# Performance work log

Measured on AMD Instinct MI355X. Metric: run time of the kernel, lower is better.

Reference implementation:

```python
import jax, jax.numpy as jnp
import numpy as np

EMBED_DIM = 1024
NUM_HEADS = 16
D_K = EMBED_DIM // NUM_HEADS


def setup_inputs() -> dict:
    key = jax.random.key(0)
    ks = jax.random.split(key, 5)
    x = jax.random.normal(ks[0], (2, 2048, EMBED_DIM), dtype=jnp.float32)
    # kaiming_normal on 2D params: std = sqrt(2/fan_in) with fan_in = in_features
    w_qkv = jax.random.normal(ks[1], (3 * EMBED_DIM, EMBED_DIM), dtype=jnp.float32) * np.sqrt(2.0 / EMBED_DIM)
    b_qkv = jnp.zeros((3 * EMBED_DIM,), dtype=jnp.float32)
    w_o = jax.random.normal(ks[2], (EMBED_DIM, EMBED_DIM), dtype=jnp.float32) * np.sqrt(2.0 / EMBED_DIM)
    b_o = jnp.zeros((EMBED_DIM,), dtype=jnp.float32)
    return {"x": x, "w_qkv": w_qkv, "b_qkv": b_qkv, "w_o": w_o, "b_o": b_o}


def reference(x, w_qkv, b_qkv, w_o, b_o):
    B, N, C = x.shape
    qkv = x @ w_qkv.T + b_qkv  # [B,N,3C]
    q, k, v = jnp.split(qkv, 3, axis=-1)
    # [B,H,N,d_k]
    q = q.reshape(B, N, NUM_HEADS, D_K).transpose(0, 2, 1, 3)
    k = k.reshape(B, N, NUM_HEADS, D_K).transpose(0, 2, 1, 3)
    v = v.reshape(B, N, NUM_HEADS, D_K).transpose(0, 2, 1, 3)
    # NOTE: original forward scales by 1/sqrt(embed_dim), not 1/sqrt(d_k)
    scores = jnp.einsum('bhqd,bhkd->bhqk', q, k) / np.sqrt(C).astype(np.float32)
    causal = jnp.tril(jnp.ones((N, N), dtype=bool))
    scores = jnp.where(causal, scores, -jnp.inf)
    attn = jax.nn.softmax(scores, axis=-1)
    out = jnp.einsum('bhqk,bhkd->bhqd', attn, v)  # [B,H,N,d_k]
    out = out.transpose(0, 2, 1, 3).reshape(B, N, C)
    return out @ w_o.T + b_o
```

## Files before the change

kernel.cpp:

```cpp
#include <hip/hip_runtime.h>
#include <hip/hip_bf16.h>
#include <math.h>

typedef __bf16 bf16_t;
typedef __bf16 bf16x8 __attribute__((ext_vector_type(8)));
typedef __bf16 bf16x4 __attribute__((ext_vector_type(4)));
typedef __bf16 bf16x2 __attribute__((ext_vector_type(2)));
typedef float f32x4 __attribute__((ext_vector_type(4)));
typedef unsigned u32x4 __attribute__((ext_vector_type(4)));

#define SCALE_L2E 0.045084234f
#define ROUND_B 0.0028169f

#define MFMA16(a, b, c) __builtin_amdgcn_mfma_f32_16x16x32_bf16(a, b, c, 0, 0, 0)

__device__ __forceinline__ unsigned pack2(float a, float b) {
  return __builtin_amdgcn_perm(__builtin_bit_cast(unsigned, b),
                               __builtin_bit_cast(unsigned, a), 0x07060302u);
}

__global__ void convert3_f32_bf16(const float* __restrict__ a, int na,
                                  const float* __restrict__ b, int nb,
                                  const float* __restrict__ c, int nc,
                                  bf16_t* __restrict__ oa, bf16_t* __restrict__ ob,
                                  bf16_t* __restrict__ oc) {
  int i = (blockIdx.x * blockDim.x + threadIdx.x) * 8;
  const float* src;
  bf16_t* dst;
  int off;
  if (i < na) { src = a; dst = oa; off = i; }
  else if (i < na + nb) { src = b; dst = ob; off = i - na; }
  else if (i < na + nb + nc) { src = c; dst = oc; off = i - na - nb; }
  else return;
  float4 u = *(const float4*)&src[off];
  float4 v = *(const float4*)&src[off + 4];
  bf16x8 w = {(bf16_t)u.x, (bf16_t)u.y, (bf16_t)u.z, (bf16_t)u.w,
              (bf16_t)v.x, (bf16_t)v.y, (bf16_t)v.z, (bf16_t)v.w};
  *(bf16x8*)&dst[off] = w;
}

#define GLOBAL_AS __attribute__((address_space(1)))
#define LDS_AS __attribute__((address_space(3)))
__device__ __forceinline__ void g2l16(const void* g, void* l) {
  __builtin_amdgcn_global_load_lds((const GLOBAL_AS void*)g, (LDS_AS void*)l,
                                   16, 0, 0);
}

template <typename TC, int BN>
__launch_bounds__(256)
__global__ void gemm_bt_bias(const bf16_t* __restrict__ A,
                             const bf16_t* __restrict__ B,
                             const float* __restrict__ bias,
                             TC* __restrict__ C,
                             int M, int N, int K) {
  constexpr int NT = BN / 32;
  __shared__ bf16_t As[128 * 32];
  __shared__ bf16_t Bs[BN * 32];

  const int t = threadIdx.x;
  const int wave = t >> 6, lane = t & 63, quad = lane >> 4, ln = lane & 15;
  const int wm = (wave >> 1) * 64, wn = (wave & 1) * (BN / 2);
  const int m0 = blockIdx.y * 128, n0 = blockIdx.x * BN;

  const int srow = lane >> 2;
  const int schunk = ((lane & 3) ^ ((lane >> 3) & 3)) * 8;
  const bf16_t* gA0 = &A[(size_t)(m0 + wave * 32 + srow) * K + schunk];
  const bf16_t* gA1 = gA0 + (size_t)16 * K;
  bf16_t* lA0 = &As[(wave * 32) * 32];
  bf16_t* lA1 = &As[(wave * 32 + 16) * 32];
  const bf16_t* gB0 = &B[(size_t)(n0 + (BN == 128 ? wave * 32 : wave * 16) + srow) * K + schunk];
  const bf16_t* gB1 = gB0 + (size_t)16 * K;
  bf16_t* lB0 = &Bs[((BN == 128 ? wave * 32 : wave * 16)) * 32];
  bf16_t* lB1 = &Bs[(wave * 32 + 16) * 32];

  const int cslot = (quad ^ ((ln >> 1) & 3)) * 8;

  f32x4 acc[4][NT];
  for (int i = 0; i < 4; i++)
    for (int j = 0; j < NT; j++) acc[i][j] = (f32x4){0.f, 0.f, 0.f, 0.f};

  for (int k0 = 0; k0 < K; k0 += 32) {
    __syncthreads();
    g2l16(gA0 + k0, lA0);
    g2l16(gA1 + k0, lA1);
    g2l16(gB0 + k0, lB0);
    if (BN == 128) g2l16(gB1 + k0, lB1);
    __syncthreads();

    bf16x8 af[4], bfr[NT];
    for (int mt = 0; mt < 4; mt++)
      af[mt] = *(const bf16x8*)&As[(wm + mt * 16 + ln) * 32 + cslot];
    for (int nt = 0; nt < NT; nt++)
      bfr[nt] = *(const bf16x8*)&Bs[(wn + nt * 16 + ln) * 32 + cslot];
    for (int mt = 0; mt < 4; mt++)
      for (int nt = 0; nt < NT; nt++)
        acc[mt][nt] = MFMA16(af[mt], bfr[nt], acc[mt][nt]);
  }

  for (int nt = 0; nt < NT; nt++) {
    int col = n0 + wn + nt * 16 + ln;
    float bv = bias[col];
    for (int mt = 0; mt < 4; mt++) {
      int row = m0 + wm + mt * 16 + quad * 4;
      for (int r = 0; r < 4; r++)
        C[(size_t)(row + r) * N + col] = (TC)(acc[mt][nt][r] + bv);
    }
  }
}

__launch_bounds__(256, 2)
__global__ void attn_kernel(const bf16_t* __restrict__ qkv,
                            bf16_t* __restrict__ out) {
  constexpr int KP = 72, VP = 72;
  constexpr int BUF = 64 * KP;
  __shared__ __align__(16) bf16_t KsB[2 * BUF];
  __shared__ __align__(16) bf16_t VtB[2 * BUF];

  const int t = threadIdx.x;
  const int wave = t >> 6, lane = t & 63, quad = lane >> 4, ln = lane & 15;
  const int p = blockIdx.x & 15;
  const int bh = blockIdx.x >> 4;
  const int b = bh >> 4, h = bh & 15;
  const int qA = p * 64, qB = (31 - p) * 64;
  const int ntiles = 32 - p;
  const size_t rs = 3072;
  const size_t base = (size_t)b * 2048 * rs;

  const size_t qoffA = base + (size_t)(qA + wave * 16 + ln) * rs + h * 64;
  const size_t qoffB = base + (size_t)(qB + wave * 16 + ln) * rs + h * 64;
  bf16x8 qfA0 = *(const bf16x8*)&qkv[qoffA + quad * 8];
  bf16x8 qfA1 = *(const bf16x8*)&qkv[qoffA + 32 + quad * 8];
  bf16x8 qfB0 = *(const bf16x8*)&qkv[qoffB + quad * 8];
  bf16x8 qfB1 = *(const bf16x8*)&qkv[qoffB + 32 + quad * 8];

  f32x4 oA[4], oB[4];
  float lAx = 0.f, lBx = 0.f;
  for (int ct = 0; ct < 4; ct++) {
    oA[ct] = (f32x4){0.f, 0.f, 0.f, 0.f};
    oB[ct] = (f32x4){0.f, 0.f, 0.f, 0.f};
  }

  const int r0 = t >> 3, c0 = (t & 7) * 8;
  const int ksA = r0 * KP + (((t & 7) + wave) & 7) * 8;
  const int ksB2 = (r0 + 32) * KP + (((t & 7) + wave + 4) & 7) * 8;
  const int vkoff = ((((r0 >> 2) + (t & 7)) & 7)) * 8 + 2 * (r0 & 3);

  const bf16_t* kpa = &qkv[base + 1024 + h * 64 + (size_t)r0 * rs + c0];
  const bf16_t* kpb = kpa + (size_t)32 * rs;
  const bf16_t* vpa = &qkv[base + 2048 + h * 64 + (size_t)(2 * r0) * rs + c0];
  const bf16_t* vpb = vpa + rs;
  const size_t tstep = (size_t)64 * rs;

  bf16x8 ka = *(const bf16x8*)kpa; kpa += tstep;
  bf16x8 kb = *(const bf16x8*)kpb; kpb += tstep;
  bf16x8 va2 = *(const bf16x8*)vpa; vpa += tstep;
  bf16x8 vb2 = *(const bf16x8*)vpb; vpb += tstep;

  const int qgA = qA + wave * 16 + ln;
  const int qgB = qB + wave * 16 + ln;

  auto stage_to = [&](int buf) {
    bf16_t* KsW = &KsB[buf * BUF];
    bf16_t* VtW = &VtB[buf * BUF];
    *(bf16x8*)&KsW[ksA] = ka;
    *(bf16x8*)&KsW[ksB2] = kb;
#pragma unroll
    for (int j = 0; j < 8; j++) {
      bf16x2 w2 = {va2[j], vb2[j]};
      *(bf16x2*)&VtW[(c0 + j) * VP + vkoff] = w2;
    }
  };
  auto prefetch = [&]() {
    ka = *(const bf16x8*)kpa; kpa += tstep;
    kb = *(const bf16x8*)kpb; kpb += tstep;
    va2 = *(const bf16x8*)vpa; vpa += tstep;
    vb2 = *(const bf16x8*)vpb; vpb += tstep;
  };
  auto load_kfs = [&](const bf16_t* Ks, bf16x8* kf0s, bf16x8* kf1s) {
#pragma unroll
    for (int st = 0; st < 4; st++) {
      const int krow = st * 16 + ln;
      const int rot = 2 * st + (ln >> 3);
      kf0s[st] = *(const bf16x8*)&Ks[krow * KP + ((quad + rot) & 7) * 8];
      kf1s[st] = *(const bf16x8*)&Ks[krow * KP + ((quad + 4 + rot) & 7) * 8];
    }
  };
  auto qk_block = [&](const bf16x8* kf0s, const bf16x8* kf1s, bf16x8 q0,
                      bf16x8 q1, float& lx, bf16x8* Bp, bool masked,
                      int kbase, int qg) {
#pragma unroll
    for (int pr = 0; pr < 2; pr++) {
      u32x4 u;
#pragma unroll
      for (int sh = 0; sh < 2; sh++) {
        const int st = pr * 2 + sh;
        f32x4 s = (f32x4){0.f, 0.f, 0.f, 0.f};
        s = MFMA16(kf0s[st], q0, s);
        s = MFMA16(kf1s[st], q1, s);
        const int k0g = kbase + st * 16 + quad * 4;
        float pv[4];
#pragma unroll
        for (int r = 0; r < 4; r++) {
          float e = __builtin_amdgcn_exp2f(fmaf(s[r], SCALE_L2E, ROUND_B));
          if (masked && (k0g + r > qg)) e = 0.f;
          lx += e;
          pv[r] = e;
        }
        u[sh * 2] = pack2(pv[0], pv[1]);
        u[sh * 2 + 1] = pack2(pv[2], pv[3]);
      }
      Bp[pr] = __builtin_bit_cast(bf16x8, u);
    }
  };
  auto load_vfs = [&](const bf16_t* Vt, bf16x8* A8s) {
#pragma unroll
    for (int pr = 0; pr < 2; pr++) {
#pragma unroll
      for (int ct = 0; ct < 4; ct++) {
        const int dd = ct * 16 + ln;
        const int bc = (quad >> 1) + 2 * ct + (ln >> 3);
        const int cA = (4 * pr + bc) & 7;
        const int cB = (4 * pr + 2 + bc) & 7;
        bf16x4 v0 = *(const bf16x4*)&Vt[dd * VP + cA * 8 + (quad & 1) * 4];
        bf16x4 v1 = *(const bf16x4*)&Vt[dd * VP + cB * 8 + (quad & 1) * 4];
        A8s[pr * 4 + ct] = __builtin_shufflevector(v0, v1, 0, 1, 2, 3, 4, 5, 6, 7);
      }
    }
  };

  auto body = [&](int kt, bool hasA, bool maskA, bool maskB) {
    if (kt + 1 < ntiles) {
      stage_to((kt + 1) & 1);
      if (kt + 2 < ntiles) prefetch();
    }
    const bf16_t* Ks = &KsB[(kt & 1) * BUF];
    const bf16_t* Vt = &VtB[(kt & 1) * BUF];
    bf16x8 kf0s[4], kf1s[4];
    load_kfs(Ks, kf0s, kf1s);
    bf16x8 BpA[2], BpB[2];
    if (hasA) qk_block(kf0s, kf1s, qfA0, qfA1, lAx, BpA, maskA, kt * 64, qgA);
    qk_block(kf0s, kf1s, qfB0, qfB1, lBx, BpB, maskB, kt * 64, qgB);
    bf16x8 A8s[8];
    load_vfs(Vt, A8s);
#pragma unroll
    for (int pr = 0; pr < 2; pr++) {
#pragma unroll
      for (int ct = 0; ct < 4; ct++) {
        if (hasA) oA[ct] = MFMA16(A8s[pr * 4 + ct], BpA[pr], oA[ct]);
        oB[ct] = MFMA16(A8s[pr * 4 + ct], BpB[pr], oB[ct]);
      }
    }
    if (kt + 1 < ntiles) __syncthreads();
  };

  stage_to(0);
  if (ntiles > 1) prefetch();
  __syncthreads();

  for (int kt = 0; kt < p; kt++) body(kt, true, false, false);
  body(p, true, true, false);
  for (int kt = p + 1; kt < 31 - p; kt++) body(kt, false, false, false);
  body(31 - p, false, false, true);

  lAx += __shfl_xor(lAx, 16);
  lAx += __shfl_xor(lAx, 32);
  lBx += __shfl_xor(lBx, 16);
  lBx += __shfl_xor(lBx, 32);
  const float invA = __builtin_amdgcn_rcpf(lAx);
  const float invB = __builtin_amdgcn_rcpf(lBx);
  const int ocol = h * 64 + quad * 4;
#pragma unroll
  for (int ct = 0; ct < 4; ct++) {
    bf16x4 wa, wb;
#pragma unroll
    for (int r = 0; r < 4; r++) {
      wa[r] = (bf16_t)(oA[ct][r] * invA);
      wb[r] = (bf16_t)(oB[ct][r] * invB);
    }
    *(bf16x4*)&out[(size_t)(b * 2048 + qgA) * 1024 + ocol + ct * 16] = wa;
    *(bf16x4*)&out[(size_t)(b * 2048 + qgB) * 1024 + ocol + ct * 16] = wb;
  }
}

extern "C" void kernel_launch(void* const* d_in, const int* in_sizes, int n_in,
                              void* d_out, int out_size, void* d_ws, size_t ws_size,
                              hipStream_t stream) {
  const float* x     = (const float*)d_in[0];
  const float* w_qkv = (const float*)d_in[1];
  const float* b_qkv = (const float*)d_in[2];
  const float* w_o   = (const float*)d_in[3];
  const float* b_o   = (const float*)d_in[4];
  float* out = (float*)d_out;

  bf16_t* qkv   = (bf16_t*)d_ws;
  bf16_t* xbf   = qkv + (size_t)4096 * 3072;
  bf16_t* wqkvb = xbf + (size_t)4096 * 1024;
  bf16_t* wob   = wqkvb + (size_t)3072 * 1024;
  bf16_t* attn  = xbf;

  const int na = 4096 * 1024, nb = 3072 * 1024, nc = 1024 * 1024;
  convert3_f32_bf16<<<dim3((na + nb + nc) / (256 * 8)), 256, 0, stream>>>(
      x, na, w_qkv, nb, w_o, nc, xbf, wqkvb, wob);

  gemm_bt_bias<bf16_t, 128><<<dim3(3072 / 128, 4096 / 128), 256, 0, stream>>>(
      xbf, wqkvb, b_qkv, qkv, 4096, 3072, 1024);
  attn_kernel<<<dim3(512), 256, 0, stream>>>(qkv, attn);
  gemm_bt_bias<float, 64><<<dim3(1024 / 64, 4096 / 128), 256, 0, stream>>>(
      attn, wob, b_o, out, 4096, 1024, 1024);
}
```

Before: 179.5 us.

## Split paired query tiles into separate blocks and compute row sums via MFMA

The attention kernel now launches one block per 64-row query tile (1024 blocks) instead of pairing tile p with tile 31-p in a single block. Blocks are ordered so short and long causal tiles interleave, and launch bounds are raised to allow more resident blocks per CU. The softmax denominator is accumulated with an extra MFMA against a vector of ones instead of scalar adds plus cross-lane shuffles. Each K/V tile is now loaded into shared memory by more blocks, and per-block work becomes uneven, which adds load imbalance and extra K/V traffic.

Result: slower. 186.1 us (+3.6%).

```diff
diff --git a/kernel.cpp b/kernel.cpp
--- a/kernel.cpp
+++ b/kernel.cpp
@@ -108,7 +108,7 @@
   }
 }
 
-__launch_bounds__(256, 2)
+__launch_bounds__(256, 4)
 __global__ void attn_kernel(const bf16_t* __restrict__ qkv,
                             bf16_t* __restrict__ out) {
   constexpr int KP = 72, VP = 72;
@@ -118,27 +118,26 @@
 
   const int t = threadIdx.x;
   const int wave = t >> 6, lane = t & 63, quad = lane >> 4, ln = lane & 15;
-  const int p = blockIdx.x & 15;
-  const int bh = blockIdx.x >> 4;
+  const int g = blockIdx.x & 255, s = blockIdx.x >> 8;
+  const int bh = g >> 3;
+  const int i = (g & 7) * 4 + s;
+  const int j = (i & 1) ? (31 - (i >> 1)) : (i >> 1);
   const int b = bh >> 4, h = bh & 15;
-  const int qA = p * 64, qB = (31 - p) * 64;
-  const int ntiles = 32 - p;
+  const int qT = j * 64;
+  const int ntiles = j + 1;
   const size_t rs = 3072;
   const size_t base = (size_t)b * 2048 * rs;
 
-  const size_t qoffA = base + (size_t)(qA + wave * 16 + ln) * rs + h * 64;
-  const size_t qoffB = base + (size_t)(qB + wave * 16 + ln) * rs + h * 64;
-  bf16x8 qfA0 = *(const bf16x8*)&qkv[qoffA + quad * 8];
-  bf16x8 qfA1 = *(const bf16x8*)&qkv[qoffA + 32 + quad * 8];
-  bf16x8 qfB0 = *(const bf16x8*)&qkv[qoffB + quad * 8];
-  bf16x8 qfB1 = *(const bf16x8*)&qkv[qoffB + 32 + quad * 8];
-
-  f32x4 oA[4], oB[4];
-  float lAx = 0.f, lBx = 0.f;
-  for (int ct = 0; ct < 4; ct++) {
-    oA[ct] = (f32x4){0.f, 0.f, 0.f, 0.f};
-    oB[ct] = (f32x4){0.f, 0.f, 0.f, 0.f};
-  }
+  const size_t qoff = base + (size_t)(qT + wave * 16 + ln) * rs + h * 64;
+  bf16x8 qf0 = *(const bf16x8*)&qkv[qoff + quad * 8];
+  bf16x8 qf1 = *(const bf16x8*)&qkv[qoff + 32 + quad * 8];
+
+  f32x4 o[4];
+  f32x4 lacc = (f32x4){0.f, 0.f, 0.f, 0.f};
+  for (int ct = 0; ct < 4; ct++) o[ct] = (f32x4){0.f, 0.f, 0.f, 0.f};
+  bf16x8 ones;
+#pragma unroll
+  for (int z = 0; z < 8; z++) ones[z] = (bf16_t)1.0f;
 
   const int r0 = t >> 3, c0 = (t & 7) * 8;
   const int ksA = r0 * KP + (((t & 7) + wave) & 7) * 8;
@@ -156,8 +155,7 @@
   bf16x8 va2 = *(const bf16x8*)vpa; vpa += tstep;
   bf16x8 vb2 = *(const bf16x8*)vpb; vpb += tstep;
 
-  const int qgA = qA + wave * 16 + ln;
-  const int qgB = qB + wave * 16 + ln;
+  const int qg = qT + wave * 16 + ln;
 
   auto stage_to = [&](int buf) {
     bf16_t* KsW = &KsB[buf * BUF];
@@ -165,9 +163,9 @@
     *(bf16x8*)&KsW[ksA] = ka;
     *(bf16x8*)&KsW[ksB2] = kb;
 #pragma unroll
-    for (int j = 0; j < 8; j++) {
-      bf16x2 w2 = {va2[j], vb2[j]};
-      *(bf16x2*)&VtW[(c0 + j) * VP + vkoff] = w2;
+    for (int z = 0; z < 8; z++) {
+      bf16x2 w2 = {va2[z], vb2[z]};
+      *(bf16x2*)&VtW[(c0 + z) * VP + vkoff] = w2;
     }
   };
   auto prefetch = [&]() {
@@ -176,34 +174,35 @@
     va2 = *(const bf16x8*)vpa; vpa += tstep;
     vb2 = *(const bf16x8*)vpb; vpb += tstep;
   };
-  auto load_kfs = [&](const bf16_t* Ks, bf16x8* kf0s, bf16x8* kf1s) {
-#pragma unroll
-    for (int st = 0; st < 4; st++) {
-      const int krow = st * 16 + ln;
-      const int rot = 2 * st + (ln >> 3);
-      kf0s[st] = *(const bf16x8*)&Ks[krow * KP + ((quad + rot) & 7) * 8];
-      kf1s[st] = *(const bf16x8*)&Ks[krow * KP + ((quad + 4 + rot) & 7) * 8];
-    }
-  };
-  auto qk_block = [&](const bf16x8* kf0s, const bf16x8* kf1s, bf16x8 q0,
-                      bf16x8 q1, float& lx, bf16x8* Bp, bool masked,
-                      int kbase, int qg) {
+
+  auto body = [&](int kt, bool masked) {
+    if (kt + 1 < ntiles) {
+      stage_to((kt + 1) & 1);
+      if (kt + 2 < ntiles) prefetch();
+    }
+    const bf16_t* Ks = &KsB[(kt & 1) * BUF];
+    const bf16_t* Vt = &VtB[(kt & 1) * BUF];
+
+    bf16x8 Bp[2];
 #pragma unroll
     for (int pr = 0; pr < 2; pr++) {
       u32x4 u;
 #pragma unroll
       for (int sh = 0; sh < 2; sh++) {
         const int st = pr * 2 + sh;
-        f32x4 s = (f32x4){0.f, 0.f, 0.f, 0.f};
-        s = MFMA16(kf0s[st], q0, s);
-        s = MFMA16(kf1s[st], q1, s);
-        const int k0g = kbase + st * 16 + quad * 4;
+        const int krow = st * 16 + ln;
+        const int rot = 2 * st + (ln >> 3);
+        bf16x8 kf0 = *(const bf16x8*)&Ks[krow * KP + ((quad + rot) & 7) * 8];
+        bf16x8 kf1 = *(const bf16x8*)&Ks[krow * KP + ((quad + 4 + rot) & 7) * 8];
+        f32x4 sc = (f32x4){0.f, 0.f, 0.f, 0.f};
+        sc = MFMA16(kf0, qf0, sc);
+        sc = MFMA16(kf1, qf1, sc);
+        const int k0g = kt * 64 + st * 16 + quad * 4;
         float pv[4];
 #pragma unroll
         for (int r = 0; r < 4; r++) {
-          float e = __builtin_amdgcn_exp2f(fmaf(s[r], SCALE_L2E, ROUND_B));
+          float e = __builtin_amdgcn_exp2f(fmaf(sc[r], SCALE_L2E, ROUND_B));
           if (masked && (k0g + r > qg)) e = 0.f;
-          lx += e;
           pv[r] = e;
         }
         u[sh * 2] = pack2(pv[0], pv[1]);
@@ -211,10 +210,10 @@
       }
       Bp[pr] = __builtin_bit_cast(bf16x8, u);
     }
-  };
-  auto load_vfs = [&](const bf16_t* Vt, bf16x8* A8s) {
+
 #pragma unroll
     for (int pr = 0; pr < 2; pr++) {
+      lacc = MFMA16(ones, Bp[pr], lacc);
 #pragma unroll
       for (int ct = 0; ct < 4; ct++) {
         const int dd = ct * 16 + ln;
@@ -223,31 +222,8 @@
         const int cB = (4 * pr + 2 + bc) & 7;
         bf16x4 v0 = *(const bf16x4*)&Vt[dd * VP + cA * 8 + (quad & 1) * 4];
         bf16x4 v1 = *(const bf16x4*)&Vt[dd * VP + cB * 8 + (quad & 1) * 4];
-        A8s[pr * 4 + ct] = __builtin_shufflevector(v0, v1, 0, 1, 2, 3, 4, 5, 6, 7);
-      }
-    }
-  };
-
-  auto body = [&](int kt, bool hasA, bool maskA, bool maskB) {
-    if (kt + 1 < ntiles) {
-      stage_to((kt + 1) & 1);
-      if (kt + 2 < ntiles) prefetch();
-    }
-    const bf16_t* Ks = &KsB[(kt & 1) * BUF];
-    const bf16_t* Vt = &VtB[(kt & 1) * BUF];
-    bf16x8 kf0s[4], kf1s[4];
-    load_kfs(Ks, kf0s, kf1s);
-    bf16x8 BpA[2], BpB[2];
-    if (hasA) qk_block(kf0s, kf1s, qfA0, qfA1, lAx, BpA, maskA, kt * 64, qgA);
-    qk_block(kf0s, kf1s, qfB0, qfB1, lBx, BpB, maskB, kt * 64, qgB);
-    bf16x8 A8s[8];
-    load_vfs(Vt, A8s);
-#pragma unroll
-    for (int pr = 0; pr < 2; pr++) {
-#pragma unroll
-      for (int ct = 0; ct < 4; ct++) {
-        if (hasA) oA[ct] = MFMA16(A8s[pr * 4 + ct], BpA[pr], oA[ct]);
-        oB[ct] = MFMA16(A8s[pr * 4 + ct], BpB[pr], oB[ct]);
+        bf16x8 A8 = __builtin_shufflevector(v0, v1, 0, 1, 2, 3, 4, 5, 6, 7);
+        o[ct] = MFMA16(A8, Bp[pr], o[ct]);
       }
     }
     if (kt + 1 < ntiles) __syncthreads();
@@ -257,28 +233,17 @@
   if (ntiles > 1) prefetch();
   __syncthreads();
 
-  for (int kt = 0; kt < p; kt++) body(kt, true, false, false);
-  body(p, true, true, false);
-  for (int kt = p + 1; kt < 31 - p; kt++) body(kt, false, false, false);
-  body(31 - p, false, false, true);
-
-  lAx += __shfl_xor(lAx, 16);
-  lAx += __shfl_xor(lAx, 32);
-  lBx += __shfl_xor(lBx, 16);
-  lBx += __shfl_xor(lBx, 32);
-  const float invA = __builtin_amdgcn_rcpf(lAx);
-  const float invB = __builtin_amdgcn_rcpf(lBx);
+  for (int kt = 0; kt < ntiles - 1; kt++) body(kt, false);
+  body(ntiles - 1, true);
+
+  const float inv = __builtin_amdgcn_rcpf(lacc[0]);
   const int ocol = h * 64 + quad * 4;
 #pragma unroll
   for (int ct = 0; ct < 4; ct++) {
-    bf16x4 wa, wb;
-#pragma unroll
-    for (int r = 0; r < 4; r++) {
-      wa[r] = (bf16_t)(oA[ct][r] * invA);
-      wb[r] = (bf16_t)(oB[ct][r] * invB);
-    }
-    *(bf16x4*)&out[(size_t)(b * 2048 + qgA) * 1024 + ocol + ct * 16] = wa;
-    *(bf16x4*)&out[(size_t)(b * 2048 + qgB) * 1024 + ocol + ct * 16] = wb;
+    bf16x4 w;
+#pragma unroll
+    for (int r = 0; r < 4; r++) w[r] = (bf16_t)(o[ct][r] * inv);
+    *(bf16x4*)&out[(size_t)(b * 2048 + qg) * 1024 + ocol + ct * 16] = w;
   }
 }
 
@@ -304,7 +269,7 @@
 
   gemm_bt_bias<bf16_t, 128><<<dim3(3072 / 128, 4096 / 128), 256, 0, stream>>>(
       xbf, wqkvb, b_qkv, qkv, 4096, 3072, 1024);
-  attn_kernel<<<dim3(512), 256, 0, stream>>>(qkv, attn);
+  attn_kernel<<<dim3(1024), 256, 0, stream>>>(qkv, attn);
   gemm_bt_bias<float, 64><<<dim3(1024 / 64, 4096 / 128), 256, 0, stream>>>(
       attn, wob, b_o, out, 4096, 1024, 1024);
 }
```

## Double GEMM K-tile to 64 with new XOR-swizzled LDS layout

Applied to the files above, without the earlier changes.

The bias GEMM now stages a 64-wide K slice per iteration instead of 32. This halves the number of __syncthreads pairs and loop iterations per output tile. The LDS layout is rewritten with an 8-chunk XOR swizzle and matching read offsets for the two MFMA sub-steps. LDS usage doubles, which may lower occupancy, and there is still no double buffering, so load latency is exposed once per larger step.

Result: no change. 180.5 us (+0.5%).

```diff
diff --git a/kernel.cpp b/kernel.cpp
--- a/kernel.cpp
+++ b/kernel.cpp
@@ -54,47 +54,56 @@
                              TC* __restrict__ C,
                              int M, int N, int K) {
   constexpr int NT = BN / 32;
-  __shared__ bf16_t As[128 * 32];
-  __shared__ bf16_t Bs[BN * 32];
+  constexpr int BCALLS = BN / 32;
+  __shared__ bf16_t As[128 * 64];
+  __shared__ bf16_t Bs[BN * 64];
 
   const int t = threadIdx.x;
   const int wave = t >> 6, lane = t & 63, quad = lane >> 4, ln = lane & 15;
   const int wm = (wave >> 1) * 64, wn = (wave & 1) * (BN / 2);
   const int m0 = blockIdx.y * 128, n0 = blockIdx.x * BN;
 
-  const int srow = lane >> 2;
-  const int schunk = ((lane & 3) ^ ((lane >> 3) & 3)) * 8;
-  const bf16_t* gA0 = &A[(size_t)(m0 + wave * 32 + srow) * K + schunk];
-  const bf16_t* gA1 = gA0 + (size_t)16 * K;
-  bf16_t* lA0 = &As[(wave * 32) * 32];
-  bf16_t* lA1 = &As[(wave * 32 + 16) * 32];
-  const bf16_t* gB0 = &B[(size_t)(n0 + (BN == 128 ? wave * 32 : wave * 16) + srow) * K + schunk];
-  const bf16_t* gB1 = gB0 + (size_t)16 * K;
-  bf16_t* lB0 = &Bs[((BN == 128 ? wave * 32 : wave * 16)) * 32];
-  bf16_t* lB1 = &Bs[(wave * 32 + 16) * 32];
-
-  const int cslot = (quad ^ ((ln >> 1) & 3)) * 8;
+  const int rown = lane >> 3;
+  const int chunk = ((lane & 7) ^ rown) * 8;
+  const bf16_t* gA = &A[(size_t)(m0 + wave * 32 + rown) * K + chunk];
+  const bf16_t* gB =
+      &B[(size_t)(n0 + (BN == 128 ? wave * 32 : wave * 16) + rown) * K + chunk];
+  bf16_t* lA = &As[(wave * 32) * 64];
+  bf16_t* lB = &Bs[(BN == 128 ? wave * 32 : wave * 16) * 64];
+
+  const int cs0 = ((0 + quad) ^ (ln & 7)) * 8;
+  const int cs1 = ((4 + quad) ^ (ln & 7)) * 8;
 
   f32x4 acc[4][NT];
   for (int i = 0; i < 4; i++)
     for (int j = 0; j < NT; j++) acc[i][j] = (f32x4){0.f, 0.f, 0.f, 0.f};
 
-  for (int k0 = 0; k0 < K; k0 += 32) {
+  for (int k0 = 0; k0 < K; k0 += 64) {
     __syncthreads();
-    g2l16(gA0 + k0, lA0);
-    g2l16(gA1 + k0, lA1);
-    g2l16(gB0 + k0, lB0);
-    if (BN == 128) g2l16(gB1 + k0, lB1);
+#pragma unroll
+    for (int c = 0; c < 4; c++)
+      g2l16(gA + k0 + (size_t)(c * 8) * K, lA + c * 8 * 64);
+#pragma unroll
+    for (int c = 0; c < BCALLS; c++)
+      g2l16(gB + k0 + (size_t)(c * 8) * K, lB + c * 8 * 64);
     __syncthreads();
 
-    bf16x8 af[4], bfr[NT];
-    for (int mt = 0; mt < 4; mt++)
-      af[mt] = *(const bf16x8*)&As[(wm + mt * 16 + ln) * 32 + cslot];
-    for (int nt = 0; nt < NT; nt++)
-      bfr[nt] = *(const bf16x8*)&Bs[(wn + nt * 16 + ln) * 32 + cslot];
-    for (int mt = 0; mt < 4; mt++)
+#pragma unroll
+    for (int h = 0; h < 2; h++) {
+      const int cs = h ? cs1 : cs0;
+      bf16x8 af[4], bfr[NT];
+#pragma unroll
+      for (int mt = 0; mt < 4; mt++)
+        af[mt] = *(const bf16x8*)&As[(wm + mt * 16 + ln) * 64 + cs];
+#pragma unroll
       for (int nt = 0; nt < NT; nt++)
-        acc[mt][nt] = MFMA16(af[mt], bfr[nt], acc[mt][nt]);
+        bfr[nt] = *(const bf16x8*)&Bs[(wn + nt * 16 + ln) * 64 + cs];
+#pragma unroll
+      for (int mt = 0; mt < 4; mt++)
+#pragma unroll
+        for (int nt = 0; nt < NT; nt++)
+          acc[mt][nt] = MFMA16(af[mt], bfr[nt], acc[mt][nt]);
+    }
   }
 
   for (int nt = 0; nt < NT; nt++) {
```
